# Optimization experiments

Measured on AMD Instinct MI355X. Metric: run time of the kernel, lower is better.

Reference implementation:

```python
import jax, jax.numpy as jnp
import numpy as np

B, N, E = 64, 2048, 32768          # graphs, nodes/graph, edges/graph
DIM = 64
RATIO = 0.8
K1 = int(np.ceil(RATIO * N))        # 1639 nodes/graph after pool1
K2 = int(np.ceil(RATIO * K1))       # 1312 nodes/graph after pool2
NUM_CLASSES = 6


def gcn_conv(x, W, b, src, dst, valid, n):
    # GCNConv with self-loops: out = D^-1/2 (A+I) D^-1/2 (x W) + b
    xw = x @ W                                          # [n, DIM]
    deg = jnp.zeros(n, x.dtype).at[dst].add(valid) + 1.0  # in-degree incl. self-loop
    norm = valid * jax.lax.rsqrt(deg[src] * deg[dst])      # per-edge norm (0 for masked)
    agg = jnp.zeros_like(xw).at[dst].add(xw[src] * norm[:, None])
    return agg + xw / deg[:, None] + b                  # self-loop term has norm 1/deg


def topk_pool(x, p, n_graphs, n_per, k):
    # PyG TopKPooling: score = tanh(x.p/||p||); keep top-k per graph; gate x by score
    score = jnp.tanh((x @ p) / jnp.linalg.norm(p))       # [n_graphs*n_per]
    vals, idx = jax.lax.top_k(score.reshape(n_graphs, n_per), k)  # [n_graphs, k]
    xg = x.reshape(n_graphs, n_per, -1)
    sel = jnp.take_along_axis(xg, idx[..., None], axis=1)          # [n_graphs, k, DIM]
    xp = sel * vals[..., None]
    perm = (idx + (jnp.arange(n_graphs) * n_per)[:, None]).reshape(-1)  # global ids kept
    return xp.reshape(n_graphs * k, -1), perm


def global_max_mean(x, n_graphs, n_per):
    xg = x.reshape(n_graphs, n_per, -1)
    return jnp.concatenate([xg.max(axis=1), xg.mean(axis=1)], axis=1)  # [n_graphs, 2*DIM]


def forward(x, edge_index, batch, W1, b1, p1, W2, b2, p2, lin1_w, lin1_b, lin2_w, lin2_b):
    src, dst = edge_index[0], edge_index[1]
    n_total = B * N
    ones = jnp.ones(src.shape[0], x.dtype)

    x = jax.nn.relu(gcn_conv(x, W1, b1, src, dst, ones, n_total))
    x, perm = topk_pool(x, p1, B, N, K1)
    x1 = global_max_mean(x, B, K1)

    # filter_adj: reindex edges to surviving nodes; drop (mask) edges touching removed nodes
    new_id = jnp.full(n_total, -1, jnp.int32).at[perm].set(jnp.arange(B * K1, dtype=jnp.int32))
    s2, d2 = new_id[src], new_id[dst]
    valid = ((s2 >= 0) & (d2 >= 0)).astype(x.dtype)
    s2 = jnp.where(s2 >= 0, s2, 0)
    d2 = jnp.where(d2 >= 0, d2, 0)

    x = jax.nn.relu(gcn_conv(x, W2, b2, s2, d2, valid, B * K1))
    x, _ = topk_pool(x, p2, B, K1, K2)
    x2 = global_max_mean(x, B, K2)

    h = x1 + x2
    h = jax.nn.relu(h @ lin1_w + lin1_b)
    return h @ lin2_w + lin2_b                           # [B, NUM_CLASSES]


def setup_inputs():
    key = jax.random.key(0)
    ks = jax.random.split(key, 10)
    x = jax.random.normal(ks[0], (B * N, DIM), jnp.float32)
    off = (jnp.arange(B) * N)[:, None]
    src = (jax.random.randint(ks[1], (B, E), 0, N) + off).reshape(-1)
    dst = (jax.random.randint(ks[2], (B, E), 0, N) + off).reshape(-1)
    edge_index = jnp.stack([src, dst]).astype(jnp.int32)
    batch = jnp.repeat(jnp.arange(B, dtype=jnp.int32), N)
    s = 1.0 / np.sqrt(DIM)
    return {
        "x": x,
        "edge_index": edge_index,
        "batch": batch,
        "W1": jax.random.normal(ks[3], (DIM, DIM), jnp.float32) * s,
        "b1": jnp.zeros(DIM, jnp.float32),
        "p1": jax.random.normal(ks[4], (DIM,), jnp.float32) * s,
        "W2": jax.random.normal(ks[5], (DIM, DIM), jnp.float32) * s,
        "b2": jnp.zeros(DIM, jnp.float32),
        "p2": jax.random.normal(ks[6], (DIM,), jnp.float32) * s,
        "lin1_w": jax.random.normal(ks[7], (2 * DIM, DIM), jnp.float32) / np.sqrt(2 * DIM),
        "lin1_b": jnp.zeros(DIM, jnp.float32),
        "lin2_w": jax.random.normal(ks[8], (DIM, NUM_CLASSES), jnp.float32) * s,
        "lin2_b": jnp.zeros(NUM_CLASSES, jnp.float32),
    }


def reference(x, edge_index, batch, W1, b1, p1, W2, b2, p2, lin1_w, lin1_b, lin2_w, lin2_b):
    return forward(x, edge_index, batch, W1, b1, p1, W2, b2, p2, lin1_w, lin1_b, lin2_w, lin2_b)
```

## Files before the change

kernel.cpp:

```cpp
#include <hip/hip_runtime.h>
#include <hip/hip_bf16.h>
#include <cstdint>
#include <cstddef>

#define B_    64
#define N_    2048
#define E_    32768
#define DIM_  64
#define K1_   1639
#define K2_   1312
#define NTOT  (B_ * N_)
#define ETOT  (B_ * E_)
#define N2TOT (B_ * K1_)
#define NCLS  6
#define PB_   8
#define CHUNKS_ 16
#define SLICES_ 16
#define BCAP  3072
#define REG_  192

typedef short bf8 __attribute__((ext_vector_type(8)));
typedef float f4  __attribute__((ext_vector_type(4)));

static __device__ __forceinline__ float2 bf2f(unsigned u) {
    float2 r;
    r.x = __uint_as_float(u << 16);
    r.y = __uint_as_float(u & 0xFFFF0000u);
    return r;
}
static __device__ __forceinline__ unsigned f2bf(float a, float b) {
    __hip_bfloat162 h = __float22bfloat162_rn(make_float2(a, b));
    unsigned u;
    __builtin_memcpy(&u, &h, 4);
    return u;
}
static __device__ __forceinline__ unsigned short f2bf_rn(float v) {
    unsigned u = __float_as_uint(v);
    return (unsigned short)((u + 0x7FFFu + ((u >> 16) & 1u)) >> 16);
}

template<int STAGE>
__launch_bounds__(256)
__global__ void k_bucket(const int* src, const int* dst, const int* remap,
                         int* bcnt, unsigned int* blist) {
    const int LSTR = (STAGE == 1) ? 128 : 103;
    __shared__ unsigned int lb[CHUNKS_][REG_];
    __shared__ int lc[CHUNKS_];
    __shared__ int rm[N_];
    int b = blockIdx.x;
    int g = b & 63, slice = b >> 6;
    int tid = threadIdx.x;
    if (tid < CHUNKS_) lc[tid] = 0;
    if (STAGE == 2)
        for (int i = tid; i < N_; i += 256) rm[i] = remap[g * N_ + i];
    __syncthreads();
    const int ESL = E_ / SLICES_;
    const int* sp = src + (size_t)g * E_ + slice * ESL;
    const int* dp = dst + (size_t)g * E_ + slice * ESL;
    int gbase = g * ((STAGE == 1) ? N_ : K1_);
    for (int e = tid * 4; e < ESL; e += 1024) {
        int4 ss = *(const int4*)&sp[e];
        int4 dd = *(const int4*)&dp[e];
#pragma unroll
        for (int t = 0; t < 4; t++) {
            int s = (&ss.x)[t], d = (&dd.x)[t];
            if (STAGE == 2) {
                s = rm[s & (N_ - 1)]; d = rm[d & (N_ - 1)];
                if ((s | d) < 0) continue;
                s -= gbase; d -= gbase;
            } else {
                s &= (N_ - 1); d &= (N_ - 1);
            }
            int ch = d / LSTR;
            int dl = d - ch * LSTR;
            int p = atomicAdd(&lc[ch], 1);
            if (p < REG_) lb[ch][p] = ((unsigned)dl << 12) | (unsigned)s;
        }
    }
    __syncthreads();
    for (int ch = 0; ch < CHUNKS_; ch++) {
        int n = min(lc[ch], REG_);
        unsigned int* out = blist + (size_t)(g * CHUNKS_ + ch) * BCAP + slice * REG_;
        for (int i = tid; i < n; i += 256) out[i] = lb[ch][i];
    }
    if (tid < CHUNKS_) bcnt[(g * SLICES_ + slice) * CHUNKS_ + tid] = min(lc[tid], REG_);
}

template<int STAGE>
__launch_bounds__(256)
__global__ void k_sort(const int* bcnt, unsigned int* blist,
                       const float* xf, const unsigned int* xg,
                       unsigned int* xb, int* ninfo) {
    const int NL   = (STAGE == 1) ? N_ : K1_;
    const int LSTR = (STAGE == 1) ? 128 : 103;
    __shared__ int cnt[128], st[128], cur[128], cnt_s[SLICES_], stot[2];
    __shared__ float rsqv[128];
    __shared__ unsigned short sorted[BCAP];
    int b = blockIdx.x;
    int g = b & 63, ch = b >> 6;
    int tid = threadIdx.x;
    if (tid < 128) { cnt[tid] = 0; cur[tid] = 0; }
    if (tid < SLICES_) cnt_s[tid] = bcnt[(g * SLICES_ + tid) * CHUNKS_ + ch];
    __syncthreads();
    size_t bb = (size_t)(g * CHUNKS_ + ch) * BCAP;
    const unsigned int* bl = blist + bb;
    const int TOT = SLICES_ * REG_;
    for (int i = tid; i < TOT; i += 256) {
        int s = i / REG_, j = i - s * REG_;
        if (j < cnt_s[s]) atomicAdd(&cnt[bl[i] >> 12], 1);
    }
    __syncthreads();
    if (tid < 128) {
        int v = cnt[tid];
        int l64 = tid & 63;
#pragma unroll
        for (int o = 1; o < 64; o <<= 1) {
            int t = __shfl_up(v, o);
            if (l64 >= o) v += t;
        }
        st[tid] = v;
        if (l64 == 63) stot[tid >> 6] = v;
    }
    __syncthreads();
    if (tid >= 64 && tid < 128) st[tid] += stot[0];
    __syncthreads();
    for (int i = tid; i < TOT; i += 256) {
        int s = i / REG_, j = i - s * REG_;
        if (j < cnt_s[s]) {
            unsigned pk = bl[i];
            int dl = (int)(pk >> 12);
            int p = st[dl] - cnt[dl] + atomicAdd(&cur[dl], 1);
            sorted[p] = (unsigned short)(pk & 0xFFFu);
        }
    }
    __syncthreads();
    int n = st[127];
    for (int i = tid; i < n; i += 256) blist[bb + i] = ((unsigned int)sorted[i]) << 5;
    int lo = ch * LSTR;
    int nloc = min(LSTR, NL - lo);
    int gbase = g * NL;
    if (tid < nloc) {
        int node = gbase + lo + tid;
        int c = cnt[tid];
        int start = (int)bb + st[tid] - c;
        ninfo[node] = (start << 8) | min(c, 255);
        rsqv[tid] = rsqrtf((float)(c + 1));
    }
    __syncthreads();
    for (int idx = tid; idx < nloc * 32; idx += 256) {
        int nl = idx >> 5, f2 = idx & 31;
        int node = gbase + lo + nl;
        float sc = rsqv[nl];
        float2 v;
        if (STAGE == 1) v = ((const float2*)xf)[(size_t)node * 32 + f2];
        else            v = bf2f(xg[(size_t)node * 32 + f2]);
        xb[(size_t)node * 32 + f2] = f2bf(v.x * sc, v.y * sc);
    }
}

template<bool GATE>
__launch_bounds__(256)
__global__ void k_agg(const unsigned int* xb, const int* ninfo, const unsigned int* csr,
                      float* y) {
    int b = blockIdx.x;
    int xcd = b & 7, r = b >> 3;
    int graph, local;
    if (GATE) {
        graph = xcd * 8 + r / 410;
        local = (r % 410) * 4 + (threadIdx.x >> 6);
        if (local >= K1_) return;
    } else {
        graph = xcd * 8 + (r >> 9);
        local = (r & 511) * 4 + (threadIdx.x >> 6);
    }
    const int NL = GATE ? K1_ : N_;
    int node = graph * NL + local;
    int lane = threadIdx.x & 63;
    int half = lane >> 5;
    int fpos = lane & 31;
    int ni = ninfo[node];
    int cnt = ni & 255, base = ni >> 8;
    float rd = rsqrtf((float)(cnt + 1));
    float ax = 0.f, ay = 0.f, bx = 0.f, by = 0.f;
    float cx = 0.f, cy = 0.f, dx = 0.f, dy = 0.f;
    int gbase32 = graph * NL * 32;
    for (int chunk = 0; chunk < cnt; chunk += 64) {
        int nch = min(64, cnt - chunk);
        int sv = 0;
        if (lane < nch) sv = gbase32 + (int)csr[base + chunk + lane];
        int i = 0;
        for (; i + 8 <= nch; i += 8) {
            int s0 = __shfl(sv, i + half),     s1 = __shfl(sv, i + 2 + half),
                s2 = __shfl(sv, i + 4 + half), s3 = __shfl(sv, i + 6 + half);
            unsigned u0 = xb[(size_t)(s0 + fpos)];
            unsigned u1 = xb[(size_t)(s1 + fpos)];
            unsigned u2 = xb[(size_t)(s2 + fpos)];
            unsigned u3 = xb[(size_t)(s3 + fpos)];
            float2 f0 = bf2f(u0), f1 = bf2f(u1), f2 = bf2f(u2), f3 = bf2f(u3);
            ax += f0.x; ay += f0.y;
            bx += f1.x; by += f1.y;
            cx += f2.x; cy += f2.y;
            dx += f3.x; dy += f3.y;
        }
        for (; i + 4 <= nch; i += 4) {
            int s0 = __shfl(sv, i + half), s1 = __shfl(sv, i + 2 + half);
            float2 f0 = bf2f(xb[(size_t)(s0 + fpos)]);
            float2 f1 = bf2f(xb[(size_t)(s1 + fpos)]);
            ax += f0.x; ay += f0.y;
            bx += f1.x; by += f1.y;
        }
        for (; i < nch; i += 2) {
            int idx = i + half;
            int s0 = __shfl(sv, idx & 63);
            float m = (idx < nch) ? 1.f : 0.f;
            float2 f0 = bf2f(xb[(size_t)(s0 + fpos)]);
            ax += f0.x * m; ay += f0.y * m;
        }
    }
    float sx = (ax + bx) + (cx + dx), sy = (ay + by) + (cy + dy);
    sx += __shfl(sx, lane ^ 32);
    sy += __shfl(sy, lane ^ 32);
    if (half == 0) {
        float2 fs = bf2f(xb[(size_t)node * 32 + fpos]);
        float2 o;
        o.x = (sx + fs.x) * rd;
        o.y = (sy + fs.y) * rd;
        ((float2*)y)[(size_t)node * 32 + fpos] = o;
    }
}

__launch_bounds__(256)
__global__ void k_convrow(float* y, const float* W, const float* bias, const float* pvec,
                          float* score, int rows) {
    int wid  = threadIdx.x >> 6;
    int lane = threadIdx.x & 63;
    int rowbase = blockIdx.x * 64 + wid * 16;
    int q = lane >> 4, c = lane & 15;
    bf8 bh[2][4], blo[2][4];
#pragma unroll
    for (int ks = 0; ks < 2; ks++)
#pragma unroll
        for (int nt = 0; nt < 4; nt++) {
            bf8 h, l;
#pragma unroll
            for (int j = 0; j < 8; j++) {
                float wv = W[(ks * 32 + q * 8 + j) * 64 + nt * 16 + c];
                unsigned short hb = f2bf_rn(wv);
                h[j] = (short)hb;
                l[j] = (short)f2bf_rn(wv - __uint_as_float((unsigned)hb << 16));
            }
            bh[ks][nt] = h; blo[ks][nt] = l;
        }
    const float* yr = y + (size_t)(rowbase + c) * DIM_ + q * 8;
    bf8 ah[2], al[2];
#pragma unroll
    for (int ks = 0; ks < 2; ks++) {
        float4 v0 = *(const float4*)(yr + ks * 32);
        float4 v1 = *(const float4*)(yr + ks * 32 + 4);
        float vv[8] = {v0.x, v0.y, v0.z, v0.w, v1.x, v1.y, v1.z, v1.w};
        bf8 h, l;
#pragma unroll
        for (int j = 0; j < 8; j++) {
            unsigned short hb = f2bf_rn(vv[j]);
            h[j] = (short)hb;
            l[j] = (short)f2bf_rn(vv[j] - __uint_as_float((unsigned)hb << 16));
        }
        ah[ks] = h; al[ks] = l;
    }
    float pp = 0.f;
#pragma unroll
    for (int i = 0; i < DIM_; i++) pp += pvec[i] * pvec[i];
    float rpn = rsqrtf(pp);
    float dot[4] = {0.f, 0.f, 0.f, 0.f};
#pragma unroll
    for (int nt = 0; nt < 4; nt++) {
        f4 acc = {0.f, 0.f, 0.f, 0.f};
#pragma unroll
        for (int ks = 0; ks < 2; ks++) {
            acc = __builtin_amdgcn_mfma_f32_16x16x32_bf16(ah[ks], bh[ks][nt],  acc, 0, 0, 0);
            acc = __builtin_amdgcn_mfma_f32_16x16x32_bf16(ah[ks], blo[ks][nt], acc, 0, 0, 0);
            acc = __builtin_amdgcn_mfma_f32_16x16x32_bf16(al[ks], bh[ks][nt],  acc, 0, 0, 0);
        }
        float bcol = bias[nt * 16 + c];
        float pcol = pvec[nt * 16 + c];
        float st[4];
#pragma unroll
        for (int reg = 0; reg < 4; reg++) {
            float v = fmaxf(acc[reg] + bcol, 0.f);
            st[reg] = v;
            dot[reg] += v * pcol;
        }
#pragma unroll
        for (int reg = 0; reg < 4; reg++)
            y[(size_t)(rowbase + q * 4 + reg) * DIM_ + nt * 16 + c] = st[reg];
    }
#pragma unroll
    for (int m = 1; m < 16; m <<= 1) {
#pragma unroll
        for (int reg = 0; reg < 4; reg++) dot[reg] += __shfl_xor(dot[reg], m);
    }
    if (c == 0) {
#pragma unroll
        for (int reg = 0; reg < 4; reg++)
            score[rowbase + q * 4 + reg] = tanhf(dot[reg] * rpn);
    }
    (void)rows;
}

template<int STAGE>
__launch_bounds__(256)
__global__ void k_selpool(const float* score, const float* conv, int* new_id,
                          unsigned int* xg, float* part) {
    const int Nin = (STAGE == 1) ? N_ : K1_;
    const int K   = (STAGE == 1) ? K1_ : K2_;
    const int RNG = (STAGE == 1) ? (N_ / PB_) : ((K1_ + PB_ - 1) / PB_);
    __shared__ unsigned long long keys[N_];
    __shared__ int bins[256], wsum[4];
    __shared__ unsigned long long s_prefix;
    __shared__ int s_need;
    __shared__ int rnk[N_];
    __shared__ float rmx[4][64], rsm[4][64];
    int b = blockIdx.x;
    int g = b & 63, pb = b >> 6;
    int tid = threadIdx.x;
    int l64 = tid & 63, wid = tid >> 6;
    const float* sg = score + (size_t)g * Nin;
    for (int i = tid; i < N_; i += 256) {
        unsigned long long key = 0ull;
        if (i < Nin) {
            unsigned u = __float_as_uint(sg[i]);
            u = (u & 0x80000000u) ? ~u : (u | 0x80000000u);
            key = ((unsigned long long)u << 11) | (unsigned long long)(2047 - i);
        }
        keys[i] = key;
    }
    if (tid == 0) { s_need = K; s_prefix = 0ull; }
    __syncthreads();
    for (int shift = 40; shift >= 0; shift -= 8) {
        bins[tid] = 0;
        __syncthreads();
        unsigned long long pref = s_prefix;
        int need = s_need;
        int hi = shift + 8;
        for (int i = tid; i < Nin; i += 256) {
            unsigned long long k = keys[i];
            if ((k >> hi) == pref) atomicAdd(&bins[(int)((k >> shift) & 255)], 1);
        }
        __syncthreads();
        int mine = bins[tid];
        int v = mine;
#pragma unroll
        for (int o = 1; o < 64; o <<= 1) {
            int t = __shfl_down(v, o);
            if (l64 + o < 64) v += t;
        }
        if (l64 == 0) wsum[wid] = v;
        __syncthreads();
        for (int w = wid + 1; w < 4; w++) v += wsum[w];
        int nxt = v - mine;
        if (v >= need && nxt < need) {
            s_prefix = (pref << 8) | (unsigned long long)tid;
            s_need = need - nxt;
        }
        __syncthreads();
    }
    unsigned long long T = s_prefix;
    if (STAGE == 1) {
        int base8 = tid * 8;
        int loc[8];
        int c8 = 0;
#pragma unroll
        for (int j = 0; j < 8; j++) { loc[j] = c8; c8 += (keys[base8 + j] >= T) ? 1 : 0; }
        int v = c8;
#pragma unroll
        for (int o = 1; o < 64; o <<= 1) {
            int t = __shfl_up(v, o);
            if (l64 >= o) v += t;
        }
        if (l64 == 63) wsum[wid] = v;
        __syncthreads();
        int wbase = 0;
        for (int w = 0; w < wid; w++) wbase += wsum[w];
        int exc = wbase + v - c8;
#pragma unroll
        for (int j = 0; j < 8; j++) rnk[base8 + j] = exc + loc[j];
        __syncthreads();
        int i = pb * RNG + tid;
        bool keep = keys[i] >= T;
        new_id[g * N_ + i] = keep ? (g * K1_ + rnk[i]) : -1;
    }
    int R0 = pb * RNG;
    int R1 = min(R0 + RNG, Nin);
    float mx = -3.402823466e38f, sm = 0.f;
    for (int i = R0 + wid; i < R1; i += 4) {
        if (keys[i] < T) continue;
        float val = sg[i];
        float v = conv[(size_t)(g * Nin + i) * DIM_ + l64] * val;
        mx = fmaxf(mx, v);
        sm += v;
        if (STAGE == 1) {
            unsigned pk = f2bf(v, __shfl_xor(v, 1));
            if (!(l64 & 1)) xg[(size_t)(g * K1_ + rnk[i]) * 32 + (l64 >> 1)] = pk;
        }
    }
    rmx[wid][l64] = mx; rsm[wid][l64] = sm;
    __syncthreads();
    if (wid == 0) {
        mx = fmaxf(fmaxf(rmx[0][l64], rmx[1][l64]), fmaxf(rmx[2][l64], rmx[3][l64]));
        sm = rsm[0][l64] + rsm[1][l64] + rsm[2][l64] + rsm[3][l64];
        part[((size_t)(g * PB_ + pb) * 2 + 0) * 64 + l64] = mx;
        part[((size_t)(g * PB_ + pb) * 2 + 1) * 64 + l64] = sm;
    }
}

__launch_bounds__(64)
__global__ void k_head(const float* part1, const float* part2,
                       const float* l1w, const float* l1b,
                       const float* l2w, const float* l2b, float* out) {
    __shared__ float h[128];
    __shared__ float h1[64];
    int g = blockIdx.x, t = threadIdx.x;
    float mx1 = -3.402823466e38f, sm1 = 0.f, mx2 = -3.402823466e38f, sm2 = 0.f;
#pragma unroll
    for (int c = 0; c < PB_; c++) {
        mx1 = fmaxf(mx1, part1[((size_t)(g * PB_ + c) * 2 + 0) * 64 + t]);
        sm1 += part1[((size_t)(g * PB_ + c) * 2 + 1) * 64 + t];
        mx2 = fmaxf(mx2, part2[((size_t)(g * PB_ + c) * 2 + 0) * 64 + t]);
        sm2 += part2[((size_t)(g * PB_ + c) * 2 + 1) * 64 + t];
    }
    h[t]      = mx1 + mx2;
    h[t + 64] = sm1 / (float)K1_ + sm2 / (float)K2_;
    __syncthreads();
    float acc = l1b[t];
#pragma unroll 8
    for (int i = 0; i < 128; i++) acc += h[i] * l1w[i * 64 + t];
    h1[t] = fmaxf(acc, 0.0f);
    __syncthreads();
    if (t < NCLS) {
        float o = l2b[t];
#pragma unroll
        for (int i = 0; i < 64; i++) o += h1[i] * l2w[i * NCLS + t];
        out[g * NCLS + t] = o;
    }
}

extern "C" void kernel_launch(void* const* d_in, const int* in_sizes, int n_in,
                              void* d_out, int out_size, void* d_ws, size_t ws_size,
                              hipStream_t stream) {
    const float* x   = (const float*)d_in[0];
    const int*   ei  = (const int*)d_in[1];
    const int*   src = ei;
    const int*   dst = ei + ETOT;
    const float* W1  = (const float*)d_in[3];
    const float* b1  = (const float*)d_in[4];
    const float* p1  = (const float*)d_in[5];
    const float* W2  = (const float*)d_in[6];
    const float* b2  = (const float*)d_in[7];
    const float* p2  = (const float*)d_in[8];
    const float* l1w = (const float*)d_in[9];
    const float* l1b = (const float*)d_in[10];
    const float* l2w = (const float*)d_in[11];
    const float* l2b = (const float*)d_in[12];
    (void)in_sizes; (void)n_in; (void)out_size; (void)ws_size;

    char* ws = (char*)d_ws;
    size_t off = 0;
    auto alloc = [&](size_t bytes) -> void* {
        void* p = ws + off;
        off = (off + bytes + 255) & ~(size_t)255;
        return p;
    };
    float*        bufA  = (float*)       alloc((size_t)NTOT  * DIM_ * 4);
    float*        bufB  = (float*)       alloc((size_t)N2TOT * DIM_ * 4);
    unsigned int* blist = (unsigned int*)alloc((size_t)B_ * CHUNKS_ * BCAP * 4);
    unsigned int* xb    = (unsigned int*)alloc((size_t)NTOT * 32 * 4);
    int*          bcnt  = (int*)         alloc((size_t)B_ * SLICES_ * CHUNKS_ * 4);
    int*          ninfo = (int*)         alloc((size_t)NTOT * 4);
    float*        score = (float*)       alloc((size_t)NTOT * 4);
    int*          newid = (int*)         alloc((size_t)NTOT * 4);
    float*        part1 = (float*)       alloc((size_t)B_ * PB_ * 128 * 4);
    float*        part2 = (float*)       alloc((size_t)B_ * PB_ * 128 * 4);
    unsigned int* xg    = (unsigned int*)bufB;

    k_bucket<1><<<B_ * SLICES_, 256, 0, stream>>>(src, dst, nullptr, bcnt, blist);
    k_sort<1><<<B_ * CHUNKS_, 256, 0, stream>>>(bcnt, blist, x, nullptr, xb, ninfo);
    k_agg<false><<<NTOT / 4, 256, 0, stream>>>(xb, ninfo, blist, bufA);
    k_convrow<<<NTOT / 64, 256, 0, stream>>>(bufA, W1, b1, p1, score, NTOT);
    k_selpool<1><<<B_ * PB_, 256, 0, stream>>>(score, bufA, newid, xg, part1);

    k_bucket<2><<<B_ * SLICES_, 256, 0, stream>>>(src, dst, newid, bcnt, blist);
    k_sort<2><<<B_ * CHUNKS_, 256, 0, stream>>>(bcnt, blist, nullptr, xg, xb, ninfo);
    k_agg<true><<<410 * B_, 256, 0, stream>>>(xb, ninfo, blist, bufB);
    k_convrow<<<N2TOT / 64, 256, 0, stream>>>(bufB, W2, b2, p2, score, N2TOT);
    k_selpool<2><<<B_ * PB_, 256, 0, stream>>>(score, bufB, nullptr, nullptr, part2);

    k_head<<<B_, 64, 0, stream>>>(part1, part2, l1w, l1b, l2w, l2b, (float*)d_out);
}
```

Measured before the change: 335.9 us.

## Split top-k selection into per-graph threshold kernel and pooling kernel

Before, each of the 8 pooling blocks per graph redid the full radix select over all 2048 keys to find the top-k threshold. Now one block per graph computes that threshold and writes it to global memory. A second kernel reads it, and each block recomputes only the kept-node counts needed for its own range's rank prefix. This removes 8x redundant radix-select work, at the cost of an extra kernel launch and the prefix-count rescan of scores.

```diff
diff --git a/kernel.cpp b/kernel.cpp
--- a/kernel.cpp
+++ b/kernel.cpp
@@ -37,6 +37,11 @@
 static __device__ __forceinline__ unsigned short f2bf_rn(float v) {
     unsigned u = __float_as_uint(v);
     return (unsigned short)((u + 0x7FFFu + ((u >> 16) & 1u)) >> 16);
+}
+static __device__ __forceinline__ unsigned long long mk_key(float s, int i) {
+    unsigned u = __float_as_uint(s);
+    u = (u & 0x80000000u) ? ~u : (u | 0x80000000u);
+    return ((unsigned long long)u << 11) | (unsigned long long)(2047 - i);
 }
 
 template<int STAGE>
@@ -309,31 +314,17 @@
 
 template<int STAGE>
 __launch_bounds__(256)
-__global__ void k_selpool(const float* score, const float* conv, int* new_id,
-                          unsigned int* xg, float* part) {
+__global__ void k_thresh(const float* score, unsigned long long* thresh) {
     const int Nin = (STAGE == 1) ? N_ : K1_;
     const int K   = (STAGE == 1) ? K1_ : K2_;
-    const int RNG = (STAGE == 1) ? (N_ / PB_) : ((K1_ + PB_ - 1) / PB_);
     __shared__ unsigned long long keys[N_];
     __shared__ int bins[256], wsum[4];
     __shared__ unsigned long long s_prefix;
     __shared__ int s_need;
-    __shared__ int rnk[N_];
-    __shared__ float rmx[4][64], rsm[4][64];
-    int b = blockIdx.x;
-    int g = b & 63, pb = b >> 6;
-    int tid = threadIdx.x;
+    int g = blockIdx.x, tid = threadIdx.x;
     int l64 = tid & 63, wid = tid >> 6;
     const float* sg = score + (size_t)g * Nin;
-    for (int i = tid; i < N_; i += 256) {
-        unsigned long long key = 0ull;
-        if (i < Nin) {
-            unsigned u = __float_as_uint(sg[i]);
-            u = (u & 0x80000000u) ? ~u : (u | 0x80000000u);
-            key = ((unsigned long long)u << 11) | (unsigned long long)(2047 - i);
-        }
-        keys[i] = key;
-    }
+    for (int i = tid; i < Nin; i += 256) keys[i] = mk_key(sg[i], i);
     if (tid == 0) { s_need = K; s_prefix = 0ull; }
     __syncthreads();
     for (int shift = 40; shift >= 0; shift -= 8) {
@@ -364,14 +355,37 @@
         }
         __syncthreads();
     }
-    unsigned long long T = s_prefix;
+    if (tid == 0) thresh[g] = s_prefix;
+}
+
+template<int STAGE>
+__launch_bounds__(256)
+__global__ void k_pool(const float* score, const float* conv, const unsigned long long* thresh,
+                       int* new_id, unsigned int* xg, float* part) {
+    const int Nin = (STAGE == 1) ? N_ : K1_;
+    const int RNG = (STAGE == 1) ? (N_ / PB_) : ((K1_ + PB_ - 1) / PB_);
+    __shared__ int rnk[256];
+    __shared__ unsigned char keepf[256];
+    __shared__ int wsum[4], s_base[4];
+    __shared__ float rmx[4][64], rsm[4][64];
+    int b = blockIdx.x;
+    int g = b & 63, pb = b >> 6;
+    int tid = threadIdx.x;
+    int l64 = tid & 63, wid = tid >> 6;
+    const float* sg = score + (size_t)g * Nin;
+    unsigned long long T = thresh[g];
+    int R0 = pb * RNG;
+    int R1 = min(R0 + RNG, Nin);
     if (STAGE == 1) {
-        int base8 = tid * 8;
-        int loc[8];
-        int c8 = 0;
-#pragma unroll
-        for (int j = 0; j < 8; j++) { loc[j] = c8; c8 += (keys[base8 + j] >= T) ? 1 : 0; }
-        int v = c8;
+        int cb = 0;
+        for (int i = tid; i < R0; i += 256) cb += (mk_key(sg[i], i) >= T) ? 1 : 0;
+#pragma unroll
+        for (int o = 32; o; o >>= 1) cb += __shfl_down(cb, o);
+        if (l64 == 0) s_base[wid] = cb;
+        int i = R0 + tid;
+        int keep = (i < R1 && mk_key(sg[i], i) >= T) ? 1 : 0;
+        keepf[tid] = (unsigned char)keep;
+        int v = keep;
 #pragma unroll
         for (int o = 1; o < 64; o <<= 1) {
             int t = __shfl_up(v, o);
@@ -379,28 +393,27 @@
         }
         if (l64 == 63) wsum[wid] = v;
         __syncthreads();
+        int base = s_base[0] + s_base[1] + s_base[2] + s_base[3];
         int wbase = 0;
         for (int w = 0; w < wid; w++) wbase += wsum[w];
-        int exc = wbase + v - c8;
-#pragma unroll
-        for (int j = 0; j < 8; j++) rnk[base8 + j] = exc + loc[j];
-        __syncthreads();
-        int i = pb * RNG + tid;
-        bool keep = keys[i] >= T;
-        new_id[g * N_ + i] = keep ? (g * K1_ + rnk[i]) : -1;
-    }
-    int R0 = pb * RNG;
-    int R1 = min(R0 + RNG, Nin);
+        int r = base + wbase + v - keep;
+        rnk[tid] = r;
+        if (i < Nin) new_id[g * N_ + i] = keep ? (g * K1_ + r) : -1;
+    } else {
+        int i = R0 + tid;
+        keepf[tid] = (unsigned char)((i < R1 && mk_key(sg[i], i) >= T) ? 1 : 0);
+    }
+    __syncthreads();
     float mx = -3.402823466e38f, sm = 0.f;
     for (int i = R0 + wid; i < R1; i += 4) {
-        if (keys[i] < T) continue;
+        if (!keepf[i - R0]) continue;
         float val = sg[i];
         float v = conv[(size_t)(g * Nin + i) * DIM_ + l64] * val;
         mx = fmaxf(mx, v);
         sm += v;
         if (STAGE == 1) {
             unsigned pk = f2bf(v, __shfl_xor(v, 1));
-            if (!(l64 & 1)) xg[(size_t)(g * K1_ + rnk[i]) * 32 + (l64 >> 1)] = pk;
+            if (!(l64 & 1)) xg[(size_t)(g * K1_ + rnk[i - R0]) * 32 + (l64 >> 1)] = pk;
         }
     }
     rmx[wid][l64] = mx; rsm[wid][l64] = sm;
@@ -470,29 +483,32 @@
         off = (off + bytes + 255) & ~(size_t)255;
         return p;
     };
-    float*        bufA  = (float*)       alloc((size_t)NTOT  * DIM_ * 4);
-    float*        bufB  = (float*)       alloc((size_t)N2TOT * DIM_ * 4);
-    unsigned int* blist = (unsigned int*)alloc((size_t)B_ * CHUNKS_ * BCAP * 4);
-    unsigned int* xb    = (unsigned int*)alloc((size_t)NTOT * 32 * 4);
-    int*          bcnt  = (int*)         alloc((size_t)B_ * SLICES_ * CHUNKS_ * 4);
-    int*          ninfo = (int*)         alloc((size_t)NTOT * 4);
-    float*        score = (float*)       alloc((size_t)NTOT * 4);
-    int*          newid = (int*)         alloc((size_t)NTOT * 4);
-    float*        part1 = (float*)       alloc((size_t)B_ * PB_ * 128 * 4);
-    float*        part2 = (float*)       alloc((size_t)B_ * PB_ * 128 * 4);
-    unsigned int* xg    = (unsigned int*)bufB;
+    float*              bufA   = (float*)             alloc((size_t)NTOT  * DIM_ * 4);
+    float*              bufB   = (float*)             alloc((size_t)N2TOT * DIM_ * 4);
+    unsigned int*       blist  = (unsigned int*)      alloc((size_t)B_ * CHUNKS_ * BCAP * 4);
+    unsigned int*       xb     = (unsigned int*)      alloc((size_t)NTOT * 32 * 4);
+    int*                bcnt   = (int*)               alloc((size_t)B_ * SLICES_ * CHUNKS_ * 4);
+    int*                ninfo  = (int*)               alloc((size_t)NTOT * 4);
+    float*              score  = (float*)             alloc((size_t)NTOT * 4);
+    int*                newid  = (int*)               alloc((size_t)NTOT * 4);
+    unsigned long long* thr    = (unsigned long long*)alloc((size_t)B_ * 8);
+    float*              part1  = (float*)             alloc((size_t)B_ * PB_ * 128 * 4);
+    float*              part2  = (float*)             alloc((size_t)B_ * PB_ * 128 * 4);
+    unsigned int*       xg     = (unsigned int*)bufB;
 
     k_bucket<1><<<B_ * SLICES_, 256, 0, stream>>>(src, dst, nullptr, bcnt, blist);
     k_sort<1><<<B_ * CHUNKS_, 256, 0, stream>>>(bcnt, blist, x, nullptr, xb, ninfo);
     k_agg<false><<<NTOT / 4, 256, 0, stream>>>(xb, ninfo, blist, bufA);
     k_convrow<<<NTOT / 64, 256, 0, stream>>>(bufA, W1, b1, p1, score, NTOT);
-    k_selpool<1><<<B_ * PB_, 256, 0, stream>>>(score, bufA, newid, xg, part1);
+    k_thresh<1><<<B_, 256, 0, stream>>>(score, thr);
+    k_pool<1><<<B_ * PB_, 256, 0, stream>>>(score, bufA, thr, newid, xg, part1);
 
     k_bucket<2><<<B_ * SLICES_, 256, 0, stream>>>(src, dst, newid, bcnt, blist);
     k_sort<2><<<B_ * CHUNKS_, 256, 0, stream>>>(bcnt, blist, nullptr, xg, xb, ninfo);
     k_agg<true><<<410 * B_, 256, 0, stream>>>(xb, ninfo, blist, bufB);
     k_convrow<<<N2TOT / 64, 256, 0, stream>>>(bufB, W2, b2, p2, score, N2TOT);
-    k_selpool<2><<<B_ * PB_, 256, 0, stream>>>(score, bufB, nullptr, nullptr, part2);
+    k_thresh<2><<<B_, 256, 0, stream>>>(score, thr);
+    k_pool<2><<<B_ * PB_, 256, 0, stream>>>(score, bufB, thr, nullptr, nullptr, part2);
 
     k_head<<<B_, 64, 0, stream>>>(part1, part2, l1w, l1b, l2w, l2b, (float*)d_out);
 }
```

After: 337.6 us. No clear change (+0.5%).
